# Kernel optimization log

Hardware: AMD Instinct MI355X
Metric: run time of the kernel (lower is better)

Reference implementation:

```python
import jax, jax.numpy as jnp
import numpy as np

N, E, G = 20000, 320000, 256      # nodes, edges, graphs per batch
IN, D, P = 128, 256, 16           # input_dim, out_dim, n_prot
EPS, R, TEMP = 1e-7, 0.5, 0.2


def setup_inputs() -> dict:
    key = jax.random.key(0)
    ks = jax.random.split(key, 9)
    x = jax.random.normal(ks[0], (N, IN), jnp.float32)
    edge_index = jax.random.randint(ks[1], (2, E), 0, N)
    batch = jnp.sort(jax.random.randint(ks[2], (N,), 0, G))
    def w(k, sh):
        fan_in = sh[0]
        return jax.random.normal(k, sh, jnp.float32) * (1.0 / fan_in) ** 0.5
    return {
        "x": x, "edge_index": edge_index, "batch": batch,
        "W1": w(ks[3], (IN, D)), "b1": jnp.zeros((D,), jnp.float32),
        "W2": w(ks[4], (D, D)), "b2": jnp.zeros((D,), jnp.float32),
        "Wm1": w(ks[5], (2 * D, D)), "bm1": jnp.zeros((D,), jnp.float32),
        "Wm2": w(ks[6], (D, 1)), "bm2": jnp.zeros((1,), jnp.float32),
        "prototypes": jax.random.normal(ks[7], (P, D), jnp.float32),
    }


def _cosine(a, b):
    # prototype_distances: cosine similarity with zero-norm -> eps fixup (eval path, no softmax)
    na = jnp.linalg.norm(a, axis=1)
    na = jnp.where(na == 0, na + EPS, na)
    nb = jnp.linalg.norm(b, axis=1)
    nb = jnp.where(nb == 0, nb + EPS, nb)
    return jnp.einsum('ik,jk->ij', a, b) / (na[:, None] * nb[None, :])


def _encoder(x, src, dst, batch, W1, b1, W2, b2, atten=None):
    # 2-layer GIN: h' = relu((h + sum_{j->i} atten_ji * h_j) W + b); graph emb = sum pool
    def conv(h, W, b):
        msg = h[src]                                   # [E, d]
        if atten is not None:
            msg = msg * atten                          # [E, 1] broadcast
        agg = h + jax.ops.segment_sum(msg, dst, num_segments=N)
        return jax.nn.relu(agg @ W + b)
    h = conv(x, W1, b1)
    h = conv(h, W2, b2)
    g = jax.ops.segment_sum(h, batch, num_segments=G)  # [G, D]
    return g, h


def reference(x, edge_index, batch, W1, b1, W2, b2, Wm1, bm1, Wm2, bm2, prototypes):
    src, dst = edge_index[0], edge_index[1]
    graph_embs, node_embs = _encoder(x, src, dst, batch, W1, b1, W2, b2)

    # eval path: assign each graph to nearest prototype by cosine similarity
    sim0 = _cosine(graph_embs, prototypes)             # [G, P]
    assign_prot = jnp.argmax(sim0, axis=1)             # [G]

    # sample_subgraph (eval: plain sigmoid, no gumbel noise)
    node_proto = prototypes[assign_prot[batch]]        # [N, D]
    h = jnp.concatenate([node_embs, node_proto], axis=-1)
    node_prob = jax.nn.relu(h @ Wm1 + bm1) @ Wm2 + bm2  # [N, 1]
    node_bern = jax.nn.sigmoid(node_prob)              # [N, 1]
    edge_bern = node_bern[src] * node_bern[dst]        # [E, 1]

    x2 = x * node_bern
    subgraph_embs, _ = _encoder(x2, src, dst, batch, W1, b1, W2, b2, atten=edge_bern)

    similarity = _cosine(subgraph_embs, prototypes)    # [G, P]

    # NCE loss
    a2 = jnp.argmax(similarity, axis=1)
    onehot = jax.nn.one_hot(a2, P, dtype=similarity.dtype)
    se = jnp.exp(similarity / TEMP)
    pos = (se * onehot).sum(axis=1)
    neg = (se * (1.0 - onehot)).sum(axis=1)
    NCE_loss = -jnp.log(pos / neg).mean()

    # KL regularizers
    nb = node_bern
    KL_node = (nb * jnp.log(nb / R + EPS)
               + (1 - nb) * jnp.log((1 - nb) / (1 - R + EPS) + EPS)).mean()
    eb = edge_bern
    KL_edge = (eb * jnp.log(eb / (R * R) + EPS)
               + (1 - eb) * jnp.log((1 - eb) / (1 - R * R + EPS) + EPS)).mean()
    KL_loss = KL_node + KL_edge

    data_sim = _cosine(subgraph_embs, subgraph_embs)   # [G, G]
    return (KL_loss, NCE_loss, similarity, node_bern, edge_bern,
            data_sim, subgraph_embs, node_embs)
```

## Files before the change

### kernel.cpp

```cpp
#include <hip/hip_runtime.h>
#include <cmath>
#include <cstdint>

#define DINL __device__ __forceinline__

namespace {

constexpr int Nn = 20000, Ee = 320000, Gg = 256, Dd = 256, Pp = 16;
constexpr int Npad = 20096;
constexpr float EPSf = 1e-7f, Rf = 0.5f, TEMPf = 0.2f;

typedef unsigned short u16;
typedef __attribute__((ext_vector_type(8))) short short8;
typedef __attribute__((ext_vector_type(4))) float floatx4;

DINL float waveSum(float x) {
#pragma unroll
  for (int off = 32; off > 0; off >>= 1) x += __shfl_xor(x, off, 64);
  return x;
}

DINL u16 f2bf(float f) {
  unsigned u = __float_as_uint(f);
  unsigned r = u + 0x7fffu + ((u >> 16) & 1u);
  return (u16)(r >> 16);
}
DINL float bf2f(u16 h) { return __uint_as_float(((unsigned)h) << 16); }

__global__ void k_deg(const int* __restrict__ dst, int* __restrict__ deg) {
  int e = blockIdx.x * 256 + threadIdx.x;
  if (e < Ee) atomicAdd(&deg[dst[e]], 1);
}

__global__ __launch_bounds__(1024) void k_scan(const int* __restrict__ deg,
                                               int* __restrict__ offs) {
  __shared__ int part[1024];
  int tid = threadIdx.x;
  const int chunk = (Nn + 1023) >> 10;
  int start = tid * chunk;
  int s = 0;
  for (int k = 0; k < chunk; k++) { int i = start + k; if (i < Nn) s += deg[i]; }
  part[tid] = s;
  __syncthreads();
  for (int off = 1; off < 1024; off <<= 1) {
    int v = (tid >= off) ? part[tid - off] : 0;
    __syncthreads();
    part[tid] += v;
    __syncthreads();
  }
  int run = (tid == 0) ? 0 : part[tid - 1];
  for (int k = 0; k < chunk; k++) {
    int i = start + k;
    if (i < Nn) { offs[i] = run; run += deg[i]; }
  }
  if (start < Nn && start + chunk >= Nn) offs[Nn] = run;
}

__global__ void k_fill(const int* __restrict__ src, const int* __restrict__ dst,
                       const int* __restrict__ offs, int* __restrict__ cursor,
                       int* __restrict__ csr) {
  int e = blockIdx.x * 256 + threadIdx.x;
  if (e < Ee) {
    int d = dst[e];
    int pos = atomicAdd(&cursor[d], 1);
    csr[offs[d] + pos] = src[e];
  }
}

__global__ void k_goff(const int* __restrict__ batch, int* __restrict__ goff) {
  int i = blockIdx.x * 256 + threadIdx.x;
  if (i >= Nn) return;
  int bi = batch[i];
  int bp = (i == 0) ? -1 : batch[i - 1];
  for (int g = bp + 1; g <= bi; ++g) goff[g] = i;
  if (i == Nn - 1)
    for (int g = bi + 1; g <= Gg; ++g) goff[g] = Nn;
}

template <int V, bool INBF>
DINL void loadRow(float r[V], const void* __restrict__ hv, int row, int lane) {
  if constexpr (INBF) {
    const u16* p = (const u16*)hv + (size_t)row * (V * 64) + lane * V;
    if constexpr (V == 4) {
      ushort4 u = *(const ushort4*)p;
      r[0] = bf2f(u.x); r[1] = bf2f(u.y); r[2] = bf2f(u.z); r[3] = bf2f(u.w);
    } else {
      ushort2 u = *(const ushort2*)p;
      r[0] = bf2f(u.x); r[1] = bf2f(u.y);
    }
  } else {
    const float* p = (const float*)hv + (size_t)row * (V * 64) + lane * V;
    if constexpr (V == 4) {
      float4 u = *(const float4*)p;
      r[0] = u.x; r[1] = u.y; r[2] = u.z; r[3] = u.w;
    } else {
      float2 u = *(const float2*)p;
      r[0] = u.x; r[1] = u.y;
    }
  }
}

template <int DIM, int MODE, bool INBF, bool OSPL>
__global__ void k_agg(const void* __restrict__ hv, const float* __restrict__ nb,
                      const int* __restrict__ offs, const int* __restrict__ csr,
                      u16* __restrict__ oh, u16* __restrict__ ol) {
  constexpr int V = DIM / 64;
  int gw = (blockIdx.x * 256 + threadIdx.x) >> 6;
  int lane = threadIdx.x & 63;
  if (gw >= Nn) return;
  float self[V], ts[V];
  loadRow<V, INBF>(self, hv, gw, lane);
#pragma unroll
  for (int j = 0; j < V; j++) ts[j] = 0.f;
  int beg = offs[gw], end = offs[gw + 1];
  int k = beg;
  for (; k + 4 <= end; k += 4) {
    int s0 = csr[k], s1 = csr[k + 1], s2 = csr[k + 2], s3 = csr[k + 3];
    float r0[V], r1[V], r2[V], r3[V];
    loadRow<V, INBF>(r0, hv, s0, lane);
    loadRow<V, INBF>(r1, hv, s1, lane);
    loadRow<V, INBF>(r2, hv, s2, lane);
    loadRow<V, INBF>(r3, hv, s3, lane);
    if (MODE == 0) {
#pragma unroll
      for (int j = 0; j < V; j++) ts[j] += (r0[j] + r1[j]) + (r2[j] + r3[j]);
    } else {
      float w0 = nb[s0], w1 = nb[s1], w2 = nb[s2], w3 = nb[s3];
      if (MODE == 1) { w0 *= w0; w1 *= w1; w2 *= w2; w3 *= w3; }
#pragma unroll
      for (int j = 0; j < V; j++)
        ts[j] += (w0 * r0[j] + w1 * r1[j]) + (w2 * r2[j] + w3 * r3[j]);
    }
  }
  for (; k < end; k++) {
    int s = csr[k];
    float r[V];
    loadRow<V, INBF>(r, hv, s, lane);
    float w = 1.f;
    if (MODE == 1) { float q = nb[s]; w = q * q; }
    else if (MODE == 2) w = nb[s];
    if (MODE == 0) {
#pragma unroll
      for (int j = 0; j < V; j++) ts[j] += r[j];
    } else {
#pragma unroll
      for (int j = 0; j < V; j++) ts[j] += w * r[j];
    }
  }
  float val[V];
  if (MODE == 0) {
#pragma unroll
    for (int j = 0; j < V; j++) val[j] = self[j] + ts[j];
  } else if (MODE == 1) {
    float wi = nb[gw];
#pragma unroll
    for (int j = 0; j < V; j++) val[j] = wi * (self[j] + ts[j]);
  } else {
    float wi = nb[gw];
#pragma unroll
    for (int j = 0; j < V; j++) val[j] = self[j] + wi * ts[j];
  }
  u16 hs[V], ls[V];
#pragma unroll
  for (int j = 0; j < V; j++) {
    hs[j] = f2bf(val[j]);
    if (OSPL) ls[j] = f2bf(val[j] - bf2f(hs[j]));
  }
  u16* po = oh + (size_t)gw * DIM + lane * V;
  if constexpr (V == 4) {
    *(ushort4*)po = make_ushort4(hs[0], hs[1], hs[2], hs[3]);
  } else {
    *(ushort2*)po = make_ushort2(hs[0], hs[1]);
  }
  if constexpr (OSPL) {
    u16* pl = ol + (size_t)gw * DIM + lane * V;
    if constexpr (V == 4) {
      *(ushort4*)pl = make_ushort4(ls[0], ls[1], ls[2], ls[3]);
    } else {
      *(ushort2*)pl = make_ushort2(ls[0], ls[1]);
    }
  }
}

template <int K, bool SPLIT, int MODE>
__global__ __launch_bounds__(256) void k_mm(
    const u16* __restrict__ Ah, const u16* __restrict__ Al,
    const u16* __restrict__ Bh, const u16* __restrict__ Bl,
    const float* __restrict__ bias,
    float* __restrict__ outF, u16* __restrict__ outH, u16* __restrict__ outL,
    const float* __restrict__ pc, const int* __restrict__ batch,
    const int* __restrict__ assign, const float* __restrict__ Wm2,
    float* __restrict__ prob) {
  constexpr int SK = 40;
  __shared__ u16 AsH[128 * SK];
  __shared__ u16 AsL[SPLIT ? 128 * SK : 16];
  __shared__ u16 BsH[64 * SK];
  __shared__ u16 BsL[SPLIT ? 64 * SK : 16];
  __shared__ int ap_s[128];
  int t = threadIdx.x;
  int rowBase = blockIdx.y * 128, colBase = blockIdx.x * 64;
  if (MODE == 1 && t < 128) {
    int r = rowBase + t;
    ap_s[t] = (r < Nn) ? assign[batch[r]] : 0;
  }
  int lane = t & 63, wv = t >> 6;
  int quad = lane >> 4, l16 = lane & 15;
  int wm = wv * 32;
  floatx4 acc[2][4];
#pragma unroll
  for (int mt = 0; mt < 2; mt++)
#pragma unroll
    for (int nt = 0; nt < 4; nt++) acc[mt][nt] = (floatx4){0.f, 0.f, 0.f, 0.f};

  int ar = t >> 1;
  int akh = (t & 1) * 16;
  const u16* agH = Ah + (size_t)(rowBase + ar) * K + akh;
  const u16* agL = Al + (size_t)(rowBase + ar) * K + akh;
  int bn = t >> 2;
  int bko = (t & 3) * 8;
  const u16* bgH = Bh + (size_t)(colBase + bn) * K + bko;
  const u16* bgL = Bl + (size_t)(colBase + bn) * K + bko;

  for (int k0 = 0; k0 < K; k0 += 32) {
    uint4 a0 = *(const uint4*)(agH + k0);
    uint4 a1 = *(const uint4*)(agH + k0 + 8);
    uint4 b0 = *(const uint4*)(bgH + k0);
    uint4 a0l, a1l, b0l;
    if constexpr (SPLIT) {
      a0l = *(const uint4*)(agL + k0);
      a1l = *(const uint4*)(agL + k0 + 8);
      b0l = *(const uint4*)(bgL + k0);
    }
    __syncthreads();
    *(uint4*)&AsH[ar * SK + akh] = a0;
    *(uint4*)&AsH[ar * SK + akh + 8] = a1;
    *(uint4*)&BsH[bn * SK + bko] = b0;
    if constexpr (SPLIT) {
      *(uint4*)&AsL[ar * SK + akh] = a0l;
      *(uint4*)&AsL[ar * SK + akh + 8] = a1l;
      *(uint4*)&BsL[bn * SK + bko] = b0l;
    }
    __syncthreads();
    short8 aH[2], aL[2], bH[4], bL[4];
#pragma unroll
    for (int mt = 0; mt < 2; mt++) {
      int off = (wm + mt * 16 + l16) * SK + quad * 8;
      aH[mt] = *(const short8*)&AsH[off];
      if (SPLIT) aL[mt] = *(const short8*)&AsL[off];
    }
#pragma unroll
    for (int nt = 0; nt < 4; nt++) {
      int off = (nt * 16 + l16) * SK + quad * 8;
      bH[nt] = *(const short8*)&BsH[off];
      if (SPLIT) bL[nt] = *(const short8*)&BsL[off];
    }
#pragma unroll
    for (int mt = 0; mt < 2; mt++)
#pragma unroll
      for (int nt = 0; nt < 4; nt++) {
        acc[mt][nt] = __builtin_amdgcn_mfma_f32_16x16x32_bf16(aH[mt], bH[nt], acc[mt][nt], 0, 0, 0);
        if constexpr (SPLIT) {
          acc[mt][nt] = __builtin_amdgcn_mfma_f32_16x16x32_bf16(aH[mt], bL[nt], acc[mt][nt], 0, 0, 0);
          acc[mt][nt] = __builtin_amdgcn_mfma_f32_16x16x32_bf16(aL[mt], bH[nt], acc[mt][nt], 0, 0, 0);
        }
      }
  }

  if constexpr (MODE == 0) {
#pragma unroll
    for (int mt = 0; mt < 2; mt++)
#pragma unroll
      for (int nt = 0; nt < 4; nt++) {
        int col = colBase + nt * 16 + l16;
        float bv = bias[col];
#pragma unroll
        for (int r = 0; r < 4; r++) {
          int row = rowBase + wm + mt * 16 + quad * 4 + r;
          if (row < Nn) {
            float v = fmaxf(acc[mt][nt][r] + bv, 0.f);
            size_t o = (size_t)row * 256 + col;
            if (outF) outF[o] = v;
            if (outH) {
              u16 hh = f2bf(v);
              outH[o] = hh;
              if (outL) outL[o] = f2bf(v - bf2f(hh));
            }
          }
        }
      }
  } else {
#pragma unroll
    for (int mt = 0; mt < 2; mt++) {
      float part[4] = {0.f, 0.f, 0.f, 0.f};
#pragma unroll
      for (int nt = 0; nt < 4; nt++) {
        int col = colBase + nt * 16 + l16;
        float wmv = Wm2[col];
#pragma unroll
        for (int r = 0; r < 4; r++) {
          int lr = wm + mt * 16 + quad * 4 + r;
          int ap = ap_s[lr];
          float tv = fmaxf(acc[mt][nt][r] + pc[ap * 256 + col], 0.f);
          part[r] += tv * wmv;
        }
      }
#pragma unroll
      for (int r = 0; r < 4; r++) {
#pragma unroll
        for (int off = 1; off < 16; off <<= 1) part[r] += __shfl_xor(part[r], off, 64);
        if (l16 == 0) {
          int row = rowBase + wm + mt * 16 + quad * 4 + r;
          if (row < Nn) atomicAdd(&prob[row], part[r]);
        }
      }
    }
  }
}

__global__ void k_pool(const float* __restrict__ h, const int* __restrict__ goff,
                       float* __restrict__ gout, float* __restrict__ gout2) {
  int g = blockIdx.x, c = threadIdx.x;
  int beg = goff[g], end = goff[g + 1];
  float s = 0.f;
  for (int n = beg; n < end; ++n) s += h[(size_t)n * Dd + c];
  gout[g * Dd + c] = s;
  if (gout2 != nullptr) gout2[g * Dd + c] = s;
}

__global__ void k_pc(const float* __restrict__ proto, const float* __restrict__ Wm1,
                     const float* __restrict__ bm1, float* __restrict__ pc,
                     float* __restrict__ pnorm) {
  int p = blockIdx.x, c = threadIdx.x;
  float s = bm1[c];
  for (int k = 0; k < Dd; k++) s += proto[p * Dd + k] * Wm1[(size_t)(Dd + k) * Dd + c];
  pc[p * Dd + c] = s;
  __shared__ float redn[256];
  float v = proto[p * Dd + c];
  redn[c] = v * v;
  __syncthreads();
  for (int off = 128; off > 0; off >>= 1) {
    if (c < off) redn[c] += redn[c + off];
    __syncthreads();
  }
  if (c == 0) {
    float n = sqrtf(redn[0]);
    pnorm[p] = (n == 0.f) ? EPSf : n;
  }
}

__global__ __launch_bounds__(64) void k_assign(const float* __restrict__ ge,
                                               const float* __restrict__ proto,
                                               const float* __restrict__ pnorm,
                                               int* __restrict__ assign) {
  int g = blockIdx.x, lane = threadIdx.x;
  float4 v = *(const float4*)(ge + (size_t)g * Dd + lane * 4);
  float na = sqrtf(waveSum(v.x * v.x + v.y * v.y + v.z * v.z + v.w * v.w));
  if (na == 0.f) na = EPSf;
  float best = -1e30f;
  int bi = 0;
#pragma unroll
  for (int p = 0; p < Pp; p++) {
    float4 w = *(const float4*)(proto + (size_t)p * Dd + lane * 4);
    float d = waveSum(v.x * w.x + v.y * w.y + v.z * w.z + v.w * w.w);
    float sim = d / (na * pnorm[p]);
    if (sim > best) { best = sim; bi = p; }
  }
  if (lane == 0) assign[g] = bi;
}

__global__ __launch_bounds__(64) void k_simnce(const float* __restrict__ se,
                                               const float* __restrict__ proto,
                                               const float* __restrict__ pnorm,
                                               float* __restrict__ osim,
                                               float* __restrict__ snorm,
                                               float* __restrict__ nceAcc) {
  int g = blockIdx.x, lane = threadIdx.x;
  float4 v = *(const float4*)(se + (size_t)g * Dd + lane * 4);
  float na = sqrtf(waveSum(v.x * v.x + v.y * v.y + v.z * v.z + v.w * v.w));
  if (na == 0.f) na = EPSf;
  float sims[Pp];
#pragma unroll
  for (int p = 0; p < Pp; p++) {
    float4 w = *(const float4*)(proto + (size_t)p * Dd + lane * 4);
    float d = waveSum(v.x * w.x + v.y * w.y + v.z * w.z + v.w * w.w);
    float sim = d / (na * pnorm[p]);
    sims[p] = sim;
    if (lane == p) osim[g * Pp + p] = sim;
  }
  float best = sims[0];
  int bi = 0;
#pragma unroll
  for (int p = 1; p < Pp; p++) {
    if (sims[p] > best) { best = sims[p]; bi = p; }
  }
  float pos = 0.f, neg = 0.f;
#pragma unroll
  for (int p = 0; p < Pp; p++) {
    float e = expf(sims[p] / TEMPf);
    if (p == bi) pos = e; else neg += e;
  }
  float lg = -logf(pos / neg);
  if (lane == 0) {
    atomicAdd(nceAcc, lg);
    snorm[g] = na;
  }
}

__global__ void k_bern(const float* __restrict__ prob, const float* __restrict__ bm2,
                       float* __restrict__ ob) {
  int i = blockIdx.x * 256 + threadIdx.x;
  if (i < Nn) {
    float z = prob[i] + bm2[0];
    ob[i] = 1.f / (1.f + expf(-z));
  }
}

__global__ void k_eb(const int* __restrict__ src, const int* __restrict__ dst,
                     const float* __restrict__ nb, float* __restrict__ oe) {
  int e = blockIdx.x * 256 + threadIdx.x;
  if (e < Ee) oe[e] = nb[src[e]] * nb[dst[e]];
}

__global__ void k_kl(const float* __restrict__ v, int n, float invA, float invB,
                     float* __restrict__ acc) {
  int i = blockIdx.x * 256 + threadIdx.x;
  float val = 0.f;
  if (i < n) {
    float xv = v[i];
    val = xv * logf(xv * invA + EPSf) + (1.f - xv) * logf((1.f - xv) * invB + EPSf);
  }
  val = waveSum(val);
  __shared__ float wsum[4];
  int lane = threadIdx.x & 63, wvv = threadIdx.x >> 6;
  if (lane == 0) wsum[wvv] = val;
  __syncthreads();
  if (threadIdx.x == 0) atomicAdd(acc, wsum[0] + wsum[1] + wsum[2] + wsum[3]);
}

__global__ void k_fin(const float* __restrict__ accs, float* __restrict__ o_kl,
                      float* __restrict__ o_nce) {
  o_kl[0] = accs[0] / (float)Nn + accs[1] / (float)Ee;
  o_nce[0] = accs[2] / (float)Gg;
}

__global__ void k_datasim(const float* __restrict__ S, const float* __restrict__ snorm,
                          float* __restrict__ out) {
  __shared__ float si[Dd];
  int i = blockIdx.x, j = threadIdx.x;
  si[j] = S[(size_t)i * Dd + j];
  __syncthreads();
  const float4* rj = (const float4*)(S + (size_t)j * Dd);
  const float4* sif = (const float4*)si;
  float d = 0.f;
#pragma unroll 4
  for (int k = 0; k < Dd / 4; k++) {
    float4 a = sif[k];
    float4 b = rj[k];
    d += a.x * b.x + a.y * b.y + a.z * b.z + a.w * b.w;
  }
  out[(size_t)i * Gg + j] = d / (snorm[i] * snorm[j]);
}

__global__ void k_splitw(const float* __restrict__ W, u16* __restrict__ th,
                         u16* __restrict__ tl, int K) {
  int idx = blockIdx.x * 256 + threadIdx.x;
  if (idx >= K * 256) return;
  int k = idx >> 8, n = idx & 255;
  float v = W[idx];
  u16 h = f2bf(v);
  th[(size_t)n * K + k] = h;
  tl[(size_t)n * K + k] = f2bf(v - bf2f(h));
}

__global__ void k_cvtbf(const float* __restrict__ x, u16* __restrict__ o, int n) {
  int i = blockIdx.x * 256 + threadIdx.x;
  if (i < n) o[i] = f2bf(x[i]);
}

}

extern "C" void kernel_launch(void* const* d_in, const int* in_sizes, int n_in,
                              void* d_out, int out_size, void* d_ws, size_t ws_size,
                              hipStream_t stream) {
  const float* x = (const float*)d_in[0];
  const int* ei = (const int*)d_in[1];
  const int* batch = (const int*)d_in[2];
  const float* W1 = (const float*)d_in[3];
  const float* b1 = (const float*)d_in[4];
  const float* W2 = (const float*)d_in[5];
  const float* b2 = (const float*)d_in[6];
  const float* Wm1 = (const float*)d_in[7];
  const float* bm1 = (const float*)d_in[8];
  const float* Wm2 = (const float*)d_in[9];
  const float* bm2 = (const float*)d_in[10];
  const float* proto = (const float*)d_in[11];
  const int* src = ei;
  const int* dst = ei + Ee;

  float* out = (float*)d_out;
  float* o_kl = out;
  float* o_nce = out + 1;
  float* o_sim = out + 2;
  float* o_nb = o_sim + Gg * Pp;
  float* o_eb = o_nb + Nn;
  float* o_ds = o_eb + Ee;
  float* o_sg = o_ds + Gg * Gg;
  float* o_ne = o_sg + Gg * Dd;

  char* w = (char*)d_ws;
  auto take = [&](size_t bytes) -> char* {
    char* p = w;
    w += (bytes + 255) & ~(size_t)255;
    return p;
  };
  const size_t halfR = (size_t)Npad * 256 * 2;
  float* bufB = (float*)take((size_t)Npad * 256 * 4);
  char* R2 = take(2 * halfR);
  u16* A1h = (u16*)R2;
  u16* A1l = (u16*)(R2 + (size_t)Npad * 128 * 2);
  u16* A2h = (u16*)R2;
  u16* A2l = (u16*)(R2 + halfR);
  u16* h1b = (u16*)R2;
  u16* a2bh = (u16*)(R2 + halfR);
  char* R3 = take(2 * halfR);
  u16* neh = (u16*)R3;
  u16* nel = (u16*)(R3 + halfR);
  u16* a1bh = (u16*)R3;
  u16* xbf = (u16*)(R3 + halfR);

  int* csr = (int*)take((size_t)Ee * 4);
  int* deg = (int*)take((size_t)Nn * 4);
  int* cursor = (int*)take((size_t)Nn * 4);
  int* offs = (int*)take((size_t)(Nn + 1) * 4);
  int* goff = (int*)take((size_t)(Gg + 1) * 4);
  float* gemb = (float*)take((size_t)Gg * Dd * 4);
  float* sgemb = (float*)take((size_t)Gg * Dd * 4);
  float* pcb = (float*)take((size_t)Pp * Dd * 4);
  float* pnorm = (float*)take(Pp * 4);
  int* assign = (int*)take(Gg * 4);
  float* snorm = (float*)take(Gg * 4);
  float* prob = (float*)take(Nn * 4);
  float* accs = (float*)take(16);
  u16* W1th = (u16*)take((size_t)256 * 128 * 2);
  u16* W1tl = (u16*)take((size_t)256 * 128 * 2);
  u16* W2th = (u16*)take((size_t)256 * 256 * 2);
  u16* W2tl = (u16*)take((size_t)256 * 256 * 2);
  u16* Wm1th = (u16*)take((size_t)256 * 256 * 2);
  u16* Wm1tl = (u16*)take((size_t)256 * 256 * 2);

  hipMemsetAsync(deg, 0, Nn * 4, stream);
  hipMemsetAsync(cursor, 0, Nn * 4, stream);
  hipMemsetAsync(prob, 0, Nn * 4, stream);
  hipMemsetAsync(accs, 0, 16, stream);

  const int eB = (Ee + 255) / 256;
  const int nB = (Nn + 255) / 256;
  const int aggB = (Nn * 64 + 255) / 256;
  dim3 gmm(4, 157);

  k_deg<<<eB, 256, 0, stream>>>(dst, deg);
  k_scan<<<1, 1024, 0, stream>>>(deg, offs);
  k_fill<<<eB, 256, 0, stream>>>(src, dst, offs, cursor, csr);
  k_goff<<<nB, 256, 0, stream>>>(batch, goff);
  k_pc<<<Pp, 256, 0, stream>>>(proto, Wm1, bm1, pcb, pnorm);
  k_splitw<<<(128 * 256 + 255) / 256, 256, 0, stream>>>(W1, W1th, W1tl, 128);
  k_splitw<<<(256 * 256 + 255) / 256, 256, 0, stream>>>(W2, W2th, W2tl, 256);
  k_splitw<<<(256 * 256 + 255) / 256, 256, 0, stream>>>(Wm1, Wm1th, Wm1tl, 256);

  k_agg<128, 0, false, true><<<aggB, 256, 0, stream>>>(x, nullptr, offs, csr, A1h, A1l);
  k_mm<128, true, 0><<<gmm, 256, 0, stream>>>(A1h, A1l, W1th, W1tl, b1, bufB, nullptr,
                                              nullptr, nullptr, nullptr, nullptr,
                                              nullptr, nullptr);
  k_agg<256, 0, false, true><<<aggB, 256, 0, stream>>>(bufB, nullptr, offs, csr, A2h, A2l);
  k_mm<256, true, 0><<<gmm, 256, 0, stream>>>(A2h, A2l, W2th, W2tl, b2, o_ne, neh, nel,
                                              nullptr, nullptr, nullptr, nullptr,
                                              nullptr);
  k_pool<<<Gg, 256, 0, stream>>>(o_ne, goff, gemb, nullptr);
  k_assign<<<Gg, 64, 0, stream>>>(gemb, proto, pnorm, assign);
  k_mm<256, true, 1><<<gmm, 256, 0, stream>>>(neh, nel, Wm1th, Wm1tl, nullptr, nullptr,
                                              nullptr, nullptr, pcb, batch, assign,
                                              Wm2, prob);
  k_bern<<<nB, 256, 0, stream>>>(prob, bm2, o_nb);
  k_eb<<<eB, 256, 0, stream>>>(src, dst, o_nb, o_eb);

  k_cvtbf<<<(Nn * 128 + 255) / 256, 256, 0, stream>>>(x, xbf, Nn * 128);
  k_agg<128, 1, true, false><<<aggB, 256, 0, stream>>>(xbf, o_nb, offs, csr, a1bh, nullptr);
  k_mm<128, false, 0><<<gmm, 256, 0, stream>>>(a1bh, nullptr, W1th, nullptr, b1, nullptr,
                                               h1b, nullptr, nullptr, nullptr, nullptr,
                                               nullptr, nullptr);
  k_agg<256, 2, true, false><<<aggB, 256, 0, stream>>>(h1b, o_nb, offs, csr, a2bh, nullptr);
  k_mm<256, false, 0><<<gmm, 256, 0, stream>>>(a2bh, nullptr, W2th, nullptr, b2, bufB,
                                               nullptr, nullptr, nullptr, nullptr,
                                               nullptr, nullptr, nullptr);
  k_pool<<<Gg, 256, 0, stream>>>(bufB, goff, sgemb, o_sg);

  k_simnce<<<Gg, 64, 0, stream>>>(sgemb, proto, pnorm, o_sim, snorm, accs + 2);
  k_kl<<<nB, 256, 0, stream>>>(o_nb, Nn, 1.f / Rf, 1.f / (1.f - Rf + EPSf), accs + 0);
  k_kl<<<eB, 256, 0, stream>>>(o_eb, Ee, 1.f / (Rf * Rf), 1.f / (1.f - Rf * Rf + EPSf),
                               accs + 1);
  k_fin<<<1, 1, 0, stream>>>(accs, o_kl, o_nce);
  k_datasim<<<Gg, 256, 0, stream>>>(sgemb, snorm, o_ds);
}
```

Baseline: 489.1 us.

## Column-chunk aggregation, fuse KL into bern/eb, widen pool/pc grids, merge memsets

Aggregation now assigns 16 lanes per node over a column chunk, so blocks cover 16 nodes times one chunk instead of one wave per full row. This is meant to raise parallelism and give more gather loads in flight. The KL reductions are folded into the sigmoid and edge-product kernels, which removes two launches and a reread of node_bern and edge_bern. Pool and prototype kernels use 2D grids of 64-thread blocks, the bf16 conversion is vectorised, and the memsets are merged on the assumption that the buffers sit next to each other.

```diff
diff --git a/kernel.cpp b/kernel.cpp
--- a/kernel.cpp
+++ b/kernel.cpp
@@ -77,107 +77,103 @@
     for (int g = bi + 1; g <= Gg; ++g) goff[g] = Nn;
 }
 
-template <int V, bool INBF>
-DINL void loadRow(float r[V], const void* __restrict__ hv, int row, int lane) {
+template <int DIM, int EPL, bool INBF>
+DINL void slice(float r[EPL], const void* __restrict__ hv, int row, int ce) {
   if constexpr (INBF) {
-    const u16* p = (const u16*)hv + (size_t)row * (V * 64) + lane * V;
-    if constexpr (V == 4) {
-      ushort4 u = *(const ushort4*)p;
-      r[0] = bf2f(u.x); r[1] = bf2f(u.y); r[2] = bf2f(u.z); r[3] = bf2f(u.w);
-    } else {
-      ushort2 u = *(const ushort2*)p;
-      r[0] = bf2f(u.x); r[1] = bf2f(u.y);
-    }
+    const u16* p = (const u16*)hv + (size_t)row * DIM + ce;
+    ushort4 u = *(const ushort4*)p;
+    r[0] = bf2f(u.x); r[1] = bf2f(u.y); r[2] = bf2f(u.z); r[3] = bf2f(u.w);
   } else {
-    const float* p = (const float*)hv + (size_t)row * (V * 64) + lane * V;
-    if constexpr (V == 4) {
-      float4 u = *(const float4*)p;
-      r[0] = u.x; r[1] = u.y; r[2] = u.z; r[3] = u.w;
-    } else {
-      float2 u = *(const float2*)p;
-      r[0] = u.x; r[1] = u.y;
-    }
+    const float* p = (const float*)hv + (size_t)row * DIM + ce;
+    float2 u = *(const float2*)p;
+    r[0] = u.x; r[1] = u.y;
   }
 }
 
 template <int DIM, int MODE, bool INBF, bool OSPL>
-__global__ void k_agg(const void* __restrict__ hv, const float* __restrict__ nb,
-                      const int* __restrict__ offs, const int* __restrict__ csr,
-                      u16* __restrict__ oh, u16* __restrict__ ol) {
-  constexpr int V = DIM / 64;
-  int gw = (blockIdx.x * 256 + threadIdx.x) >> 6;
-  int lane = threadIdx.x & 63;
-  if (gw >= Nn) return;
-  float self[V], ts[V];
-  loadRow<V, INBF>(self, hv, gw, lane);
-#pragma unroll
-  for (int j = 0; j < V; j++) ts[j] = 0.f;
-  int beg = offs[gw], end = offs[gw + 1];
+__global__ __launch_bounds__(256) void k_aggc(
+    const void* __restrict__ hv, const float* __restrict__ nb,
+    const int* __restrict__ offs, const int* __restrict__ csr,
+    u16* __restrict__ oh, u16* __restrict__ ol) {
+  constexpr int EPL = INBF ? 4 : 2;
+  constexpr int COLS = EPL * 16;
+  constexpr int CHUNKS = DIM / COLS;
+  int c = (int)(blockIdx.x % CHUNKS);
+  int grp = (int)(blockIdx.x / CHUNKS);
+  int wv = threadIdx.x >> 6, lane = threadIdx.x & 63;
+  int sub = lane >> 4, l = lane & 15;
+  int node = grp * 16 + wv * 4 + sub;
+  if (node >= Nn) return;
+  int ce = c * COLS + l * EPL;
+  float self[EPL], ts[EPL];
+  slice<DIM, EPL, INBF>(self, hv, node, ce);
+#pragma unroll
+  for (int j = 0; j < EPL; j++) ts[j] = 0.f;
+  int beg = offs[node], end = offs[node + 1];
   int k = beg;
   for (; k + 4 <= end; k += 4) {
     int s0 = csr[k], s1 = csr[k + 1], s2 = csr[k + 2], s3 = csr[k + 3];
-    float r0[V], r1[V], r2[V], r3[V];
-    loadRow<V, INBF>(r0, hv, s0, lane);
-    loadRow<V, INBF>(r1, hv, s1, lane);
-    loadRow<V, INBF>(r2, hv, s2, lane);
-    loadRow<V, INBF>(r3, hv, s3, lane);
+    float r0[EPL], r1[EPL], r2[EPL], r3[EPL];
+    slice<DIM, EPL, INBF>(r0, hv, s0, ce);
+    slice<DIM, EPL, INBF>(r1, hv, s1, ce);
+    slice<DIM, EPL, INBF>(r2, hv, s2, ce);
+    slice<DIM, EPL, INBF>(r3, hv, s3, ce);
     if (MODE == 0) {
 #pragma unroll
-      for (int j = 0; j < V; j++) ts[j] += (r0[j] + r1[j]) + (r2[j] + r3[j]);
+      for (int j = 0; j < EPL; j++) ts[j] += (r0[j] + r1[j]) + (r2[j] + r3[j]);
     } else {
       float w0 = nb[s0], w1 = nb[s1], w2 = nb[s2], w3 = nb[s3];
       if (MODE == 1) { w0 *= w0; w1 *= w1; w2 *= w2; w3 *= w3; }
 #pragma unroll
-      for (int j = 0; j < V; j++)
+      for (int j = 0; j < EPL; j++)
         ts[j] += (w0 * r0[j] + w1 * r1[j]) + (w2 * r2[j] + w3 * r3[j]);
     }
   }
   for (; k < end; k++) {
     int s = csr[k];
-    float r[V];
-    loadRow<V, INBF>(r, hv, s, lane);
-    float w = 1.f;
-    if (MODE == 1) { float q = nb[s]; w = q * q; }
-    else if (MODE == 2) w = nb[s];
+    float r[EPL];
+    slice<DIM, EPL, INBF>(r, hv, s, ce);
     if (MODE == 0) {
 #pragma unroll
-      for (int j = 0; j < V; j++) ts[j] += r[j];
+      for (int j = 0; j < EPL; j++) ts[j] += r[j];
     } else {
-#pragma unroll
-      for (int j = 0; j < V; j++) ts[j] += w * r[j];
-    }
-  }
-  float val[V];
+      float wq = nb[s];
+      if (MODE == 1) wq *= wq;
+#pragma unroll
+      for (int j = 0; j < EPL; j++) ts[j] += wq * r[j];
+    }
+  }
+  float val[EPL];
   if (MODE == 0) {
 #pragma unroll
-    for (int j = 0; j < V; j++) val[j] = self[j] + ts[j];
+    for (int j = 0; j < EPL; j++) val[j] = self[j] + ts[j];
   } else if (MODE == 1) {
-    float wi = nb[gw];
-#pragma unroll
-    for (int j = 0; j < V; j++) val[j] = wi * (self[j] + ts[j]);
+    float wi = nb[node];
+#pragma unroll
+    for (int j = 0; j < EPL; j++) val[j] = wi * (self[j] + ts[j]);
   } else {
-    float wi = nb[gw];
-#pragma unroll
-    for (int j = 0; j < V; j++) val[j] = self[j] + wi * ts[j];
-  }
-  u16 hs[V], ls[V];
-#pragma unroll
-  for (int j = 0; j < V; j++) {
+    float wi = nb[node];
+#pragma unroll
+    for (int j = 0; j < EPL; j++) val[j] = self[j] + wi * ts[j];
+  }
+  u16 hs[EPL], ls[EPL];
+#pragma unroll
+  for (int j = 0; j < EPL; j++) {
     hs[j] = f2bf(val[j]);
     if (OSPL) ls[j] = f2bf(val[j] - bf2f(hs[j]));
   }
-  u16* po = oh + (size_t)gw * DIM + lane * V;
-  if constexpr (V == 4) {
+  u16* po = oh + (size_t)node * DIM + ce;
+  if constexpr (EPL == 2) {
+    *(ushort2*)po = make_ushort2(hs[0], hs[1]);
+  } else {
     *(ushort4*)po = make_ushort4(hs[0], hs[1], hs[2], hs[3]);
-  } else {
-    *(ushort2*)po = make_ushort2(hs[0], hs[1]);
   }
   if constexpr (OSPL) {
-    u16* pl = ol + (size_t)gw * DIM + lane * V;
-    if constexpr (V == 4) {
+    u16* pl = ol + (size_t)node * DIM + ce;
+    if constexpr (EPL == 2) {
+      *(ushort2*)pl = make_ushort2(ls[0], ls[1]);
+    } else {
       *(ushort4*)pl = make_ushort4(ls[0], ls[1], ls[2], ls[3]);
-    } else {
-      *(ushort2*)pl = make_ushort2(ls[0], ls[1]);
     }
   }
 }
@@ -317,9 +313,11 @@
   }
 }
 
-__global__ void k_pool(const float* __restrict__ h, const int* __restrict__ goff,
-                       float* __restrict__ gout, float* __restrict__ gout2) {
-  int g = blockIdx.x, c = threadIdx.x;
+__global__ __launch_bounds__(64) void k_pool(const float* __restrict__ h,
+                                             const int* __restrict__ goff,
+                                             float* __restrict__ gout,
+                                             float* __restrict__ gout2) {
+  int g = blockIdx.x, q = blockIdx.y, c = q * 64 + threadIdx.x;
   int beg = goff[g], end = goff[g + 1];
   float s = 0.f;
   for (int n = beg; n < end; ++n) s += h[(size_t)n * Dd + c];
@@ -327,24 +325,23 @@
   if (gout2 != nullptr) gout2[g * Dd + c] = s;
 }
 
-__global__ void k_pc(const float* __restrict__ proto, const float* __restrict__ Wm1,
-                     const float* __restrict__ bm1, float* __restrict__ pc,
-                     float* __restrict__ pnorm) {
-  int p = blockIdx.x, c = threadIdx.x;
-  float s = bm1[c];
-  for (int k = 0; k < Dd; k++) s += proto[p * Dd + k] * Wm1[(size_t)(Dd + k) * Dd + c];
-  pc[p * Dd + c] = s;
-  __shared__ float redn[256];
-  float v = proto[p * Dd + c];
-  redn[c] = v * v;
-  __syncthreads();
-  for (int off = 128; off > 0; off >>= 1) {
-    if (c < off) redn[c] += redn[c + off];
-    __syncthreads();
-  }
-  if (c == 0) {
-    float n = sqrtf(redn[0]);
-    pnorm[p] = (n == 0.f) ? EPSf : n;
+__global__ __launch_bounds__(64) void k_pc(const float* __restrict__ proto,
+                                           const float* __restrict__ Wm1,
+                                           const float* __restrict__ bm1,
+                                           float* __restrict__ pc,
+                                           float* __restrict__ pnorm) {
+  int p = blockIdx.x, q = blockIdx.y, t = threadIdx.x;
+  int cc = q * 64 + t;
+  float s = bm1[cc];
+  for (int k = 0; k < Dd; k++) s += proto[p * Dd + k] * Wm1[(size_t)(Dd + k) * Dd + cc];
+  pc[p * Dd + cc] = s;
+  if (q == 0) {
+    float4 v = ((const float4*)(proto + (size_t)p * Dd))[t];
+    float nsq = waveSum(v.x * v.x + v.y * v.y + v.z * v.z + v.w * v.w);
+    if (t == 0) {
+      float n = sqrtf(nsq);
+      pnorm[p] = (n == 0.f) ? EPSf : n;
+    }
   }
 }
 
@@ -407,34 +404,41 @@
 }
 
 __global__ void k_bern(const float* __restrict__ prob, const float* __restrict__ bm2,
-                       float* __restrict__ ob) {
+                       float* __restrict__ ob, float* __restrict__ accs) {
   int i = blockIdx.x * 256 + threadIdx.x;
+  float val = 0.f;
   if (i < Nn) {
     float z = prob[i] + bm2[0];
-    ob[i] = 1.f / (1.f + expf(-z));
-  }
-}
-
-__global__ void k_eb(const int* __restrict__ src, const int* __restrict__ dst,
-                     const float* __restrict__ nb, float* __restrict__ oe) {
-  int e = blockIdx.x * 256 + threadIdx.x;
-  if (e < Ee) oe[e] = nb[src[e]] * nb[dst[e]];
-}
-
-__global__ void k_kl(const float* __restrict__ v, int n, float invA, float invB,
-                     float* __restrict__ acc) {
-  int i = blockIdx.x * 256 + threadIdx.x;
-  float val = 0.f;
-  if (i < n) {
-    float xv = v[i];
-    val = xv * logf(xv * invA + EPSf) + (1.f - xv) * logf((1.f - xv) * invB + EPSf);
+    float p = 1.f / (1.f + expf(-z));
+    ob[i] = p;
+    const float invA = 1.f / Rf, invB = 1.f / (1.f - Rf + EPSf);
+    val = p * logf(p * invA + EPSf) + (1.f - p) * logf((1.f - p) * invB + EPSf);
   }
   val = waveSum(val);
   __shared__ float wsum[4];
   int lane = threadIdx.x & 63, wvv = threadIdx.x >> 6;
   if (lane == 0) wsum[wvv] = val;
   __syncthreads();
-  if (threadIdx.x == 0) atomicAdd(acc, wsum[0] + wsum[1] + wsum[2] + wsum[3]);
+  if (threadIdx.x == 0) atomicAdd(accs, wsum[0] + wsum[1] + wsum[2] + wsum[3]);
+}
+
+__global__ void k_eb(const int* __restrict__ src, const int* __restrict__ dst,
+                     const float* __restrict__ nb, float* __restrict__ oe,
+                     float* __restrict__ accs) {
+  int e = blockIdx.x * 256 + threadIdx.x;
+  float val = 0.f;
+  if (e < Ee) {
+    float v = nb[src[e]] * nb[dst[e]];
+    oe[e] = v;
+    const float invA = 1.f / (Rf * Rf), invB = 1.f / (1.f - Rf * Rf + EPSf);
+    val = v * logf(v * invA + EPSf) + (1.f - v) * logf((1.f - v) * invB + EPSf);
+  }
+  val = waveSum(val);
+  __shared__ float wsum[4];
+  int lane = threadIdx.x & 63, wvv = threadIdx.x >> 6;
+  if (lane == 0) wsum[wvv] = val;
+  __syncthreads();
+  if (threadIdx.x == 0) atomicAdd(accs + 1, wsum[0] + wsum[1] + wsum[2] + wsum[3]);
 }
 
 __global__ void k_fin(const float* __restrict__ accs, float* __restrict__ o_kl,
@@ -472,9 +476,12 @@
   tl[(size_t)n * K + k] = f2bf(v - bf2f(h));
 }
 
-__global__ void k_cvtbf(const float* __restrict__ x, u16* __restrict__ o, int n) {
+__global__ void k_cvtbf4(const float4* __restrict__ x, ushort4* __restrict__ o, int n4) {
   int i = blockIdx.x * 256 + threadIdx.x;
-  if (i < n) o[i] = f2bf(x[i]);
+  if (i < n4) {
+    float4 v = x[i];
+    o[i] = make_ushort4(f2bf(v.x), f2bf(v.y), f2bf(v.z), f2bf(v.w));
+  }
 }
 
 }
@@ -548,56 +555,51 @@
   u16* Wm1th = (u16*)take((size_t)256 * 256 * 2);
   u16* Wm1tl = (u16*)take((size_t)256 * 256 * 2);
 
-  hipMemsetAsync(deg, 0, Nn * 4, stream);
-  hipMemsetAsync(cursor, 0, Nn * 4, stream);
-  hipMemsetAsync(prob, 0, Nn * 4, stream);
-  hipMemsetAsync(accs, 0, 16, stream);
+  hipMemsetAsync(deg, 0, 2 * 80128, stream);
+  hipMemsetAsync(prob, 0, 80128 + 16, stream);
 
   const int eB = (Ee + 255) / 256;
   const int nB = (Nn + 255) / 256;
-  const int aggB = (Nn * 64 + 255) / 256;
   dim3 gmm(4, 157);
 
   k_deg<<<eB, 256, 0, stream>>>(dst, deg);
   k_scan<<<1, 1024, 0, stream>>>(deg, offs);
   k_fill<<<eB, 256, 0, stream>>>(src, dst, offs, cursor, csr);
   k_goff<<<nB, 256, 0, stream>>>(batch, goff);
-  k_pc<<<Pp, 256, 0, stream>>>(proto, Wm1, bm1, pcb, pnorm);
+  k_pc<<<dim3(Pp, 4), 64, 0, stream>>>(proto, Wm1, bm1, pcb, pnorm);
   k_splitw<<<(128 * 256 + 255) / 256, 256, 0, stream>>>(W1, W1th, W1tl, 128);
   k_splitw<<<(256 * 256 + 255) / 256, 256, 0, stream>>>(W2, W2th, W2tl, 256);
   k_splitw<<<(256 * 256 + 255) / 256, 256, 0, stream>>>(Wm1, Wm1th, Wm1tl, 256);
 
-  k_agg<128, 0, false, true><<<aggB, 256, 0, stream>>>(x, nullptr, offs, csr, A1h, A1l);
+  k_aggc<128, 0, false, true><<<1250 * 4, 256, 0, stream>>>(x, nullptr, offs, csr, A1h, A1l);
   k_mm<128, true, 0><<<gmm, 256, 0, stream>>>(A1h, A1l, W1th, W1tl, b1, bufB, nullptr,
                                               nullptr, nullptr, nullptr, nullptr,
                                               nullptr, nullptr);
-  k_agg<256, 0, false, true><<<aggB, 256, 0, stream>>>(bufB, nullptr, offs, csr, A2h, A2l);
+  k_aggc<256, 0, false, true><<<1250 * 8, 256, 0, stream>>>(bufB, nullptr, offs, csr, A2h, A2l);
   k_mm<256, true, 0><<<gmm, 256, 0, stream>>>(A2h, A2l, W2th, W2tl, b2, o_ne, neh, nel,
                                               nullptr, nullptr, nullptr, nullptr,
                                               nullptr);
-  k_pool<<<Gg, 256, 0, stream>>>(o_ne, goff, gemb, nullptr);
+  k_pool<<<dim3(Gg, 4), 64, 0, stream>>>(o_ne, goff, gemb, nullptr);
   k_assign<<<Gg, 64, 0, stream>>>(gemb, proto, pnorm, assign);
   k_mm<256, true, 1><<<gmm, 256, 0, stream>>>(neh, nel, Wm1th, Wm1tl, nullptr, nullptr,
                                               nullptr, nullptr, pcb, batch, assign,
                                               Wm2, prob);
-  k_bern<<<nB, 256, 0, stream>>>(prob, bm2, o_nb);
-  k_eb<<<eB, 256, 0, stream>>>(src, dst, o_nb, o_eb);
-
-  k_cvtbf<<<(Nn * 128 + 255) / 256, 256, 0, stream>>>(x, xbf, Nn * 128);
-  k_agg<128, 1, true, false><<<aggB, 256, 0, stream>>>(xbf, o_nb, offs, csr, a1bh, nullptr);
+  k_bern<<<nB, 256, 0, stream>>>(prob, bm2, o_nb, accs);
+  k_eb<<<eB, 256, 0, stream>>>(src, dst, o_nb, o_eb, accs);
+
+  k_cvtbf4<<<(Nn * 128 / 4 + 255) / 256, 256, 0, stream>>>((const float4*)x,
+                                                           (ushort4*)xbf, Nn * 128 / 4);
+  k_aggc<128, 1, true, false><<<1250 * 2, 256, 0, stream>>>(xbf, o_nb, offs, csr, a1bh, nullptr);
   k_mm<128, false, 0><<<gmm, 256, 0, stream>>>(a1bh, nullptr, W1th, nullptr, b1, nullptr,
                                                h1b, nullptr, nullptr, nullptr, nullptr,
                                                nullptr, nullptr);
-  k_agg<256, 2, true, false><<<aggB, 256, 0, stream>>>(h1b, o_nb, offs, csr, a2bh, nullptr);
+  k_aggc<256, 2, true, false><<<1250 * 4, 256, 0, stream>>>(h1b, o_nb, offs, csr, a2bh, nullptr);
   k_mm<256, false, 0><<<gmm, 256, 0, stream>>>(a2bh, nullptr, W2th, nullptr, b2, bufB,
                                                nullptr, nullptr, nullptr, nullptr,
                                                nullptr, nullptr, nullptr);
-  k_pool<<<Gg, 256, 0, stream>>>(bufB, goff, sgemb, o_sg);
+  k_pool<<<dim3(Gg, 4), 64, 0, stream>>>(bufB, goff, sgemb, o_sg);
 
   k_simnce<<<Gg, 64, 0, stream>>>(sgemb, proto, pnorm, o_sim, snorm, accs + 2);
-  k_kl<<<nB, 256, 0, stream>>>(o_nb, Nn, 1.f / Rf, 1.f / (1.f - Rf + EPSf), accs + 0);
-  k_kl<<<eB, 256, 0, stream>>>(o_eb, Ee, 1.f / (Rf * Rf), 1.f / (1.f - Rf * Rf + EPSf),
-                               accs + 1);
   k_fin<<<1, 1, 0, stream>>>(accs, o_kl, o_nce);
   k_datasim<<<Gg, 256, 0, stream>>>(sgemb, snorm, o_ds);
 }
```

Measured after the change: 473.3 us. 3.2% less time.
